# Performance work log

Hardware: AMD Instinct MI355X
Metric: run time of the kernel (lower is better)

Reference implementation:

```python
import jax, jax.numpy as jnp
import numpy as np

N_P, N_A, D, H, E = 200000, 100000, 64, 32, 1000000


def setup_inputs() -> dict:
    key = jax.random.key(0)
    ks = jax.random.split(key, 32)
    inp = {}
    inp["x_paper"] = jax.random.normal(ks[0], (N_P, D), jnp.float32)
    inp["x_author"] = jax.random.normal(ks[1], (N_A, D), jnp.float32)
    inp["cites_src"] = jax.random.randint(ks[2], (E,), 0, N_P, jnp.int32)
    inp["cites_dst"] = jax.random.randint(ks[3], (E,), 0, N_P, jnp.int32)
    inp["writes_src"] = jax.random.randint(ks[4], (E,), 0, N_A, jnp.int32)
    inp["writes_dst"] = jax.random.randint(ks[5], (E,), 0, N_P, jnp.int32)
    inp["rev_src"] = jax.random.randint(ks[6], (E,), 0, N_P, jnp.int32)
    inp["rev_dst"] = jax.random.randint(ks[7], (E,), 0, N_A, jnp.int32)
    # per-relation SAGEConv params; layer 1: D->H, layer 2: H->H
    i = 8
    for layer, din in ((1, D), (2, H)):
        for rel in ("cites", "writes", "rev"):
            inp[f"W{layer}l_{rel}"] = 0.1 * jax.random.normal(ks[i], (din, H), jnp.float32); i += 1
            inp[f"W{layer}r_{rel}"] = 0.1 * jax.random.normal(ks[i], (din, H), jnp.float32); i += 1
            inp[f"b{layer}_{rel}"] = 0.01 * jax.random.normal(ks[i], (H,), jnp.float32); i += 1
    return inp


def _sage(x_src, x_dst, src, dst, Wl, Wr, b, n_dst):
    # PyG SAGEConv (aggr='mean'): lin_l(mean of source msgs) + lin_r(x_dst) + bias
    msg = x_src[src]                                              # [E, d] gather
    s = jax.ops.segment_sum(msg, dst, num_segments=n_dst)         # [n_dst, d]
    cnt = jax.ops.segment_sum(jnp.ones((src.shape[0],), x_src.dtype), dst, num_segments=n_dst)
    mean = s / jnp.maximum(cnt, 1.0)[:, None]
    return mean @ Wl + x_dst @ Wr + b


def reference(x_paper, x_author, cites_src, cites_dst, writes_src, writes_dst,
              rev_src, rev_dst,
              W1l_cites, W1r_cites, b1_cites, W1l_writes, W1r_writes, b1_writes,
              W1l_rev, W1r_rev, b1_rev,
              W2l_cites, W2r_cites, b2_cites, W2l_writes, W2r_writes, b2_writes,
              W2l_rev, W2r_rev, b2_rev):
    n_p, n_a = x_paper.shape[0], x_author.shape[0]
    # layer 1 (to_hetero sums relation outputs per dst node type), then relu
    p1 = jax.nn.relu(
        _sage(x_paper, x_paper, cites_src, cites_dst, W1l_cites, W1r_cites, b1_cites, n_p)
        + _sage(x_author, x_paper, writes_src, writes_dst, W1l_writes, W1r_writes, b1_writes, n_p))
    a1 = jax.nn.relu(
        _sage(x_paper, x_author, rev_src, rev_dst, W1l_rev, W1r_rev, b1_rev, n_a))
    # layer 2, return 'paper' output (no activation)
    p2 = (_sage(p1, p1, cites_src, cites_dst, W2l_cites, W2r_cites, b2_cites, n_p)
          + _sage(a1, p1, writes_src, writes_dst, W2l_writes, W2r_writes, b2_writes, n_p))
    return p2
```

## Files before the change

kernel.cpp:

```cpp
#include <hip/hip_runtime.h>

typedef unsigned short u16;
typedef unsigned int   u32;
typedef __attribute__((ext_vector_type(8))) short bf16x8;
typedef __attribute__((ext_vector_type(4))) float f32x4;

#define N_P 200000
#define N_A 100000
#define DD  64
#define HH  32
#define NE  1000000
#define NBP 782
#define NBA 391
#define NB4K 245
#define NCB 196
#define P4CAP 8192
#define NB_P16 12500
#define NB_A16 6250

__device__ inline float bf2f(u16 u) { return __uint_as_float(((u32)u) << 16); }
__device__ inline u16 f2bf(float f) {
    u32 u = __float_as_uint(f);
    u += 0x7fffu + ((u >> 16) & 1u);
    return (u16)(u >> 16);
}
__device__ inline float lo_f(u32 m) { return __uint_as_float(m << 16); }
__device__ inline float hi_f(u32 m) { return __uint_as_float(m & 0xffff0000u); }

__device__ inline void gseg_dual(
    const u16* __restrict__ yA, const int* __restrict__ bkA, int s0, int e0,
    const u16* __restrict__ yB, const int* __restrict__ bkB, int s1, int e1,
    int lane, float& axo, float& ayo, float& bxo, float& byo) {
    float ax = 0.f, ay = 0.f, bx = 0.f, by = 0.f;
    int lastA = min(max(e0 - 1, s0), NE - 1);
    int lastB = min(max(e1 - 1, s1), NE - 1);
    for (int j0 = s0, j1 = s1; (j0 < e0) || (j1 < e1); j0 += 8, j1 += 8) {
        int ia[8], ib[8];
#pragma unroll
        for (int i = 0; i < 8; ++i) ia[i] = bkA[min(j0 + i, lastA)];
#pragma unroll
        for (int i = 0; i < 8; ++i) ib[i] = bkB[min(j1 + i, lastB)];
        u32 ma[8], mb[8];
#pragma unroll
        for (int i = 0; i < 8; ++i)
            ma[i] = *(const u32*)(yA + (size_t)(u32)ia[i] + lane * 2);
#pragma unroll
        for (int i = 0; i < 8; ++i)
            mb[i] = *(const u32*)(yB + (size_t)(u32)ib[i] + lane * 2);
#pragma unroll
        for (int i = 0; i < 8; ++i) {
            u32 va = (j0 + i < e0) ? ma[i] : 0u;
            ax += lo_f(va); ay += hi_f(va);
        }
#pragma unroll
        for (int i = 0; i < 8; ++i) {
            u32 vb = (j1 + i < e1) ? mb[i] : 0u;
            bx += lo_f(vb); by += hi_f(vb);
        }
    }
    axo = ax; ayo = ay; bxo = bx; byo = by;
}

__global__ __launch_bounds__(256) void p1_hist_k(
    const int* __restrict__ cd, const int* __restrict__ wd, const int* __restrict__ rd,
    int* __restrict__ gsizes) {
    int rel = blockIdx.y;
    const int* dst; int shift;
    if (rel == 0)      { dst = cd; shift = 10; }
    else if (rel == 1) { dst = wd; shift = 10; }
    else               { dst = rd; shift = 9;  }
    __shared__ int cnt[256];
    int t = threadIdx.x;
    cnt[t] = 0;
    __syncthreads();
    int e0 = blockIdx.x * 4096;
    if (e0 + 4096 <= NE) {
        const int4* dv = (const int4*)(dst + e0);
#pragma unroll
        for (int i = 0; i < 4; ++i) {
            int4 v = dv[i * 256 + t];
            atomicAdd(&cnt[v.x >> shift], 1);
            atomicAdd(&cnt[v.y >> shift], 1);
            atomicAdd(&cnt[v.z >> shift], 1);
            atomicAdd(&cnt[v.w >> shift], 1);
        }
    } else {
#pragma unroll
        for (int i = 0; i < 16; ++i) {
            int e = e0 + i * 256 + t;
            if (e < NE) atomicAdd(&cnt[dst[e] >> shift], 1);
        }
    }
    __syncthreads();
    if (t < NCB && cnt[t]) atomicAdd(&gsizes[rel * NCB + t], cnt[t]);
}

__global__ __launch_bounds__(256) void p2_scan_k(
    const int* __restrict__ gsizes, int* __restrict__ bases, int* __restrict__ gcur) {
    __shared__ int lds[256];
    int t = threadIdx.x;
    for (int rel = 0; rel < 3; ++rel) {
        int v = (t < NCB) ? gsizes[rel * NCB + t] : 0;
        lds[t] = v; __syncthreads();
#pragma unroll
        for (int o = 1; o < 256; o <<= 1) {
            int x = (t >= o) ? lds[t - o] : 0;
            __syncthreads();
            lds[t] += x;
            __syncthreads();
        }
        int ex = lds[t] - v;
        if (t < NCB) { bases[rel * NCB + t] = ex; gcur[rel * NCB + t] = ex; }
        __syncthreads();
    }
}

__global__ __launch_bounds__(256) void p3_bin_k(
    const int* __restrict__ cs, const int* __restrict__ cd,
    const int* __restrict__ ws_, const int* __restrict__ wd,
    const int* __restrict__ rs, const int* __restrict__ rd,
    int* __restrict__ gcur,
    u32* __restrict__ pr_c, u32* __restrict__ pr_w, u32* __restrict__ pr_r) {
    int rel = blockIdx.y;
    const int *src, *dst; int shift; u32* out;
    if (rel == 0)      { src = cs;  dst = cd; shift = 10; out = pr_c; }
    else if (rel == 1) { src = ws_; dst = wd; shift = 10; out = pr_w; }
    else               { src = rs;  dst = rd; shift = 9;  out = pr_r; }
    __shared__ u32 sbuf[4096];
    __shared__ int cnt[256], sc[256], lcur[256], gbase[256];
    int t = threadIdx.x;
    cnt[t] = 0;
    __syncthreads();
    int e0 = blockIdx.x * 4096;
    int myd[16], mys[16];
    if (e0 + 4096 <= NE) {
        const int4* dv = (const int4*)(dst + e0);
        const int4* sv = (const int4*)(src + e0);
#pragma unroll
        for (int i = 0; i < 4; ++i) {
            int4 v = dv[i * 256 + t];
            int4 s = sv[i * 256 + t];
            myd[4 * i] = v.x; myd[4 * i + 1] = v.y; myd[4 * i + 2] = v.z; myd[4 * i + 3] = v.w;
            mys[4 * i] = s.x; mys[4 * i + 1] = s.y; mys[4 * i + 2] = s.z; mys[4 * i + 3] = s.w;
            atomicAdd(&cnt[v.x >> shift], 1);
            atomicAdd(&cnt[v.y >> shift], 1);
            atomicAdd(&cnt[v.z >> shift], 1);
            atomicAdd(&cnt[v.w >> shift], 1);
        }
    } else {
#pragma unroll
        for (int i = 0; i < 4; ++i) {
#pragma unroll
            for (int c = 0; c < 4; ++c) {
                int e = e0 + (i * 256 + t) * 4 + c;
                int idx = 4 * i + c;
                if (e < NE) {
                    myd[idx] = dst[e]; mys[idx] = src[e];
                    atomicAdd(&cnt[myd[idx] >> shift], 1);
                } else { myd[idx] = -1; mys[idx] = 0; }
            }
        }
    }
    __syncthreads();
    int v = cnt[t];
    sc[t] = v; __syncthreads();
#pragma unroll
    for (int o = 1; o < 256; o <<= 1) {
        int x = (t >= o) ? sc[t - o] : 0;
        __syncthreads();
        sc[t] += x;
        __syncthreads();
    }
    int ex = sc[t] - v;
    __syncthreads();
    sc[t] = ex;
    lcur[t] = ex;
    if (t < NCB) gbase[t] = atomicAdd(&gcur[rel * NCB + t], cnt[t]);
    __syncthreads();
#pragma unroll
    for (int i = 0; i < 16; ++i) {
        if (myd[i] >= 0) {
            int d = myd[i];
            int cb = d >> shift;
            u32 dloc = (u32)(d - (cb << shift));
            u32 pk = (dloc << 18) | (u32)mys[i];
            int p = atomicAdd(&lcur[cb], 1);
            sbuf[p] = pk;
        }
    }
    __syncthreads();
    int nvalid = min(4096, NE - e0);
    for (int i = t; i < nvalid; i += 256) {
        int lo = 0, hi = NCB - 1;
        while (lo < hi) {
            int mid = (lo + hi + 1) >> 1;
            if (sc[mid] <= i) lo = mid; else hi = mid - 1;
        }
        out[gbase[lo] + (i - sc[lo])] = sbuf[i];
    }
}

__global__ __launch_bounds__(256) void p4_sort_k(
    const int* __restrict__ bases, const int* __restrict__ gsizes,
    const u32* __restrict__ pr_c, const u32* __restrict__ pr_w, const u32* __restrict__ pr_r,
    int* __restrict__ bkt_c, int* __restrict__ bkt_w, int* __restrict__ bkt_r,
    int* __restrict__ st_c, int* __restrict__ st_w, int* __restrict__ st_r) {
    int rel = blockIdx.y;
    const u32* pr; int* bkt; int* st; int width, n;
    if (rel == 0)      { pr = pr_c; bkt = bkt_c; st = st_c; width = 1024; n = N_P; }
    else if (rel == 1) { pr = pr_w; bkt = bkt_w; st = st_w; width = 1024; n = N_P; }
    else               { pr = pr_r; bkt = bkt_r; st = st_r; width = 512;  n = N_A; }
    __shared__ u32 sin[P4CAP];
    __shared__ int cnt[1024], sc2[1024], tmp[256];
    int t = threadIdx.x;
    int b = blockIdx.x;
    int base = bases[rel * NCB + b];
    int size = min(gsizes[rel * NCB + b], P4CAP);
    int d0 = b * width;
    int nd = min(width, n - d0);
    if (nd <= 0) return;
#pragma unroll
    for (int j = t; j < 1024; j += 256) cnt[j] = 0;
    __syncthreads();
    for (int i = t; i < size; i += 256) {
        u32 pk = pr[base + i];
        sin[i] = pk;
        atomicAdd(&cnt[pk >> 18], 1);
    }
    __syncthreads();
    int j0 = 4 * t;
    int c0 = cnt[j0], c1 = cnt[j0 + 1], c2 = cnt[j0 + 2], c3 = cnt[j0 + 3];
    int tot = c0 + c1 + c2 + c3;
    tmp[t] = tot; __syncthreads();
#pragma unroll
    for (int o = 1; o < 256; o <<= 1) {
        int x = (t >= o) ? tmp[t - o] : 0;
        __syncthreads();
        tmp[t] += x;
        __syncthreads();
    }
    int pre = tmp[t] - tot;
    sc2[j0] = pre;
    sc2[j0 + 1] = pre + c0;
    sc2[j0 + 2] = pre + c0 + c1;
    sc2[j0 + 3] = pre + c0 + c1 + c2;
    __syncthreads();
    for (int j = t; j < nd; j += 256) st[d0 + j] = base + sc2[j];
#pragma unroll
    for (int j = t; j < 1024; j += 256) cnt[j] = 0;
    __syncthreads();
    for (int i = t; i < size; i += 256) {
        u32 pk = sin[i];
        int dl = (int)(pk >> 18);
        int pos = sc2[dl] + atomicAdd(&cnt[dl], 1);
        bkt[base + pos] = (int)((pk & 0x3FFFFu) * HH);
    }
}

__global__ __launch_bounds__(256) void prep_w_k(
    const float* __restrict__ W1lc, const float* __restrict__ W1lr,
    const float* __restrict__ W1rc, const float* __restrict__ W1rw,
    const float* __restrict__ W1lw, const float* __restrict__ W1rr,
    const float* __restrict__ W2lc, const float* __restrict__ W2rc,
    const float* __restrict__ W2rw, const float* __restrict__ W2lw,
    const float* __restrict__ b1c, const float* __restrict__ b1w,
    const float* __restrict__ b2c, const float* __restrict__ b2w,
    u16* __restrict__ wt1h, u16* __restrict__ wt1l,
    u16* __restrict__ wt2h, u16* __restrict__ wt2l,
    float* __restrict__ b1s, float* __restrict__ b2s,
    int* __restrict__ gsizes) {
    int m = blockIdx.x, t = threadIdx.x;
    if (m == 0) {
        for (int e = t; e < 3 * NCB; e += 256) gsizes[e] = 0;
    }
    if (m < 5) {
        const float *A = nullptr, *B = nullptr;
        if (m == 0) A = W1lc;
        else if (m == 1) A = W1lr;
        else if (m == 2) { A = W1rc; B = W1rw; }
        else if (m == 3) A = W1lw;
        else A = W1rr;
        for (int e = t; e < 2048; e += 256) {
            int k = e >> 5, n = e & 31;
            float v = A[e] + (B ? B[e] : 0.f);
            u16 h = f2bf(v);
            u16 lw = f2bf(v - bf2f(h));
            wt1h[m * 2048 + n * 64 + k] = h;
            wt1l[m * 2048 + n * 64 + k] = lw;
        }
        if (m == 2 && t < HH) b1s[t] = b1c[t] + b1w[t];
    } else {
        int mm = m - 5;
        const float *A = nullptr, *B = nullptr;
        if (mm == 0) A = W2lc;
        else if (mm == 1) { A = W2rc; B = W2rw; }
        else A = W2lw;
        for (int e = t; e < 1024; e += 256) {
            int k = e >> 5, n = e & 31;
            float v = A[e] + (B ? B[e] : 0.f);
            u16 h = f2bf(v);
            u16 lw = f2bf(v - bf2f(h));
            wt2h[mm * 1024 + n * 32 + k] = h;
            wt2l[mm * 1024 + n * 32 + k] = lw;
        }
        if (mm == 1 && t < HH) b2s[t] = b2c[t] + b2w[t];
    }
}

__global__ __launch_bounds__(256) void t1_k(
    const float* __restrict__ xp, const float* __restrict__ xa,
    const u16* __restrict__ wt1h, const u16* __restrict__ wt1l,
    const float* __restrict__ b1s, const float* __restrict__ b1r,
    u16* __restrict__ y_pc, u16* __restrict__ y_pr, u16* __restrict__ y_aw,
    u16* __restrict__ hb_p, u16* __restrict__ hb_a) {
    __shared__ float Cs[256 * 34];
    int t = threadIdx.x, w = t >> 6, l = t & 63;
    int lm = l & 15, lk = l >> 4;
    bool paper = blockIdx.x < NBP;
    int row0 = (paper ? blockIdx.x : blockIdx.x - NBP) * 256;
    const float* x = paper ? xp : xa;
    int NROW = paper ? N_P : N_A;
    int nv = min(256, NROW - row0);
    bf16x8 xh[4][2], xl[4][2];
#pragma unroll
    for (int i = 0; i < 4; ++i) {
        int rowg = min(row0 + w * 64 + i * 16 + lm, NROW - 1);
        const float* rp = x + (size_t)rowg * DD + lk * 8;
#pragma unroll
        for (int kc = 0; kc < 2; ++kc) {
            float4 a = *(const float4*)(rp + kc * 32);
            float4 b = *(const float4*)(rp + kc * 32 + 4);
            float f[8] = {a.x, a.y, a.z, a.w, b.x, b.y, b.z, b.w};
            union { u32 u[4]; bf16x8 v; } H, L;
#pragma unroll
            for (int j = 0; j < 4; ++j) {
                u16 h0 = f2bf(f[2 * j]), h1 = f2bf(f[2 * j + 1]);
                float l0 = f[2 * j] - bf2f(h0), l1 = f[2 * j + 1] - bf2f(h1);
                H.u[j] = (u32)h0 | ((u32)h1 << 16);
                L.u[j] = (u32)f2bf(l0) | ((u32)f2bf(l1) << 16);
            }
            xh[i][kc] = H.v; xl[i][kc] = L.v;
        }
    }
    int nw = paper ? 3 : 2;
#pragma unroll 1
    for (int iw = 0; iw < nw; ++iw) {
        int mat = paper ? iw : (3 + iw);
        const u16* Wh = wt1h + mat * 2048;
        const u16* Wl = wt1l + mat * 2048;
        bf16x8 Bh[2][2], Bl[2][2];
#pragma unroll
        for (int ct = 0; ct < 2; ++ct)
#pragma unroll
            for (int kc = 0; kc < 2; ++kc) {
                int off = (ct * 16 + lm) * 64 + kc * 32 + lk * 8;
                Bh[ct][kc] = *(const bf16x8*)(Wh + off);
                Bl[ct][kc] = *(const bf16x8*)(Wl + off);
            }
        float bv[2] = {0.f, 0.f};
        if (paper && iw == 2)  { bv[0] = b1s[lm]; bv[1] = b1s[16 + lm]; }
        if (!paper && iw == 1) { bv[0] = b1r[lm]; bv[1] = b1r[16 + lm]; }
#pragma unroll
        for (int i = 0; i < 4; ++i) {
#pragma unroll
            for (int ct = 0; ct < 2; ++ct) {
                f32x4 acc = {bv[ct], bv[ct], bv[ct], bv[ct]};
                acc = __builtin_amdgcn_mfma_f32_16x16x32_bf16(xh[i][0], Bh[ct][0], acc, 0, 0, 0);
                acc = __builtin_amdgcn_mfma_f32_16x16x32_bf16(xh[i][1], Bh[ct][1], acc, 0, 0, 0);
                acc = __builtin_amdgcn_mfma_f32_16x16x32_bf16(xl[i][0], Bh[ct][0], acc, 0, 0, 0);
                acc = __builtin_amdgcn_mfma_f32_16x16x32_bf16(xl[i][1], Bh[ct][1], acc, 0, 0, 0);
                acc = __builtin_amdgcn_mfma_f32_16x16x32_bf16(xh[i][0], Bl[ct][0], acc, 0, 0, 0);
                acc = __builtin_amdgcn_mfma_f32_16x16x32_bf16(xh[i][1], Bl[ct][1], acc, 0, 0, 0);
                int rbase = w * 64 + i * 16 + lk * 4;
#pragma unroll
                for (int r = 0; r < 4; ++r)
                    Cs[(rbase + r) * 34 + ct * 16 + lm] = acc[r];
            }
        }
        asm volatile("s_waitcnt lgkmcnt(0)" ::: "memory");
        u16* outp;
        if (paper) outp = (iw == 0) ? y_pc : (iw == 1) ? y_pr : hb_p;
        else       outp = (iw == 0) ? y_aw : hb_a;
        u32* g = (u32*)(outp + (size_t)row0 * HH);
#pragma unroll
        for (int p = 0; p < 4; ++p) {
            int j = p * 64 + l;
            int rl = w * 64 + (j >> 2);
            if (rl < nv) {
                const float* q = Cs + rl * 34 + (j & 3) * 8;
                u32 o[4];
#pragma unroll
                for (int jj = 0; jj < 4; ++jj)
                    o[jj] = (u32)f2bf(q[2 * jj]) | ((u32)f2bf(q[2 * jj + 1]) << 16);
                *(uint4*)(g + ((size_t)w * 256 + j) * 4) = make_uint4(o[0], o[1], o[2], o[3]);
            }
        }
        asm volatile("" ::: "memory");
    }
}

__global__ __launch_bounds__(256) void agg1_k(
    const u16* __restrict__ y_pc, const u16* __restrict__ y_aw,
    const u16* __restrict__ y_pr,
    const int* __restrict__ st_c, const int* __restrict__ bkt_c,
    const int* __restrict__ st_w, const int* __restrict__ bkt_w,
    const int* __restrict__ st_r, const int* __restrict__ bkt_r,
    u32* __restrict__ hb_p, u32* __restrict__ hb_a) {
    int t = threadIdx.x, g = t >> 4, lane = t & 15;
    if (blockIdx.x < NB_P16) {
        int row = blockIdx.x * 16 + g;
        int s0 = st_c[row];
        int e0 = (row == N_P - 1) ? NE : st_c[row + 1];
        int s1 = st_w[row];
        int e1 = (row == N_P - 1) ? NE : st_w[row + 1];
        float cx, cy, wx, wy;
        gseg_dual(y_pc, bkt_c, s0, e0, y_aw, bkt_w, s1, e1, lane, cx, cy, wx, wy);
        int d0 = e0 - s0, d1 = e1 - s1;
        float iv0 = 1.0f / (float)(d0 < 1 ? 1 : d0);
        float iv1 = 1.0f / (float)(d1 < 1 ? 1 : d1);
        u32 self = hb_p[(size_t)row * (HH / 2) + lane];
        float ax = cx * iv0 + wx * iv1 + lo_f(self);
        float ay = cy * iv0 + wy * iv1 + hi_f(self);
        hb_p[(size_t)row * (HH / 2) + lane] = (u32)f2bf(ax) | ((u32)f2bf(ay) << 16);
    } else {
        int row = (blockIdx.x - NB_P16) * 16 + g;
        int s = st_r[row];
        int e = (row == N_A - 1) ? NE : st_r[row + 1];
        int mid = (s + e) >> 1;
        float ax0, ay0, ax1, ay1;
        gseg_dual(y_pr, bkt_r, s, mid, y_pr, bkt_r, mid, e, lane, ax0, ay0, ax1, ay1);
        int dg = e - s;
        float iv = 1.0f / (float)(dg < 1 ? 1 : dg);
        u32 self = hb_a[(size_t)row * (HH / 2) + lane];
        float ax = (ax0 + ax1) * iv + lo_f(self);
        float ay = (ay0 + ay1) * iv + hi_f(self);
        hb_a[(size_t)row * (HH / 2) + lane] = (u32)f2bf(ax) | ((u32)f2bf(ay) << 16);
    }
}

__global__ __launch_bounds__(256) void t2_k(
    const u32* __restrict__ hb_p, const u32* __restrict__ hb_a,
    const u16* __restrict__ wt2h, const u16* __restrict__ wt2l,
    const float* __restrict__ b2s,
    u16* __restrict__ z_p, u16* __restrict__ z_a, float* __restrict__ hp2) {
    __shared__ float Cs[256 * 34];
    int t = threadIdx.x, w = t >> 6, l = t & 63;
    int lm = l & 15, lk = l >> 4;
    bool paper = blockIdx.x < NBP;
    int row0 = (paper ? blockIdx.x : blockIdx.x - NBP) * 256;
    const u32* hb = paper ? hb_p : hb_a;
    int NROW = paper ? N_P : N_A;
    int nv = min(256, NROW - row0);
    bf16x8 af[4];
#pragma unroll
    for (int i = 0; i < 4; ++i) {
        int rowg = min(row0 + w * 64 + i * 16 + lm, NROW - 1);
        uint4 q = *(const uint4*)(hb + (size_t)rowg * (HH / 2) + lk * 4);
        u32 qq[4] = {q.x, q.y, q.z, q.w};
        union { u32 u[4]; bf16x8 v; } A;
#pragma unroll
        for (int j = 0; j < 4; ++j) {
            u32 m = ((qq[j] & 0x80008000u) >> 15) * 0xFFFFu;
            A.u[j] = qq[j] & ~m;
        }
        af[i] = A.v;
    }
    int nw = paper ? 2 : 1;
#pragma unroll 1
    for (int iw = 0; iw < nw; ++iw) {
        int mat = paper ? iw : 2;
        const u16* Wh = wt2h + mat * 1024;
        const u16* Wl = wt2l + mat * 1024;
        bf16x8 Bh[2], Bl[2];
#pragma unroll
        for (int ct = 0; ct < 2; ++ct) {
            int off = (ct * 16 + lm) * 32 + lk * 8;
            Bh[ct] = *(const bf16x8*)(Wh + off);
            Bl[ct] = *(const bf16x8*)(Wl + off);
        }
        float bv[2] = {0.f, 0.f};
        if (paper && iw == 1) { bv[0] = b2s[lm]; bv[1] = b2s[16 + lm]; }
#pragma unroll
        for (int i = 0; i < 4; ++i) {
#pragma unroll
            for (int ct = 0; ct < 2; ++ct) {
                f32x4 acc = {bv[ct], bv[ct], bv[ct], bv[ct]};
                acc = __builtin_amdgcn_mfma_f32_16x16x32_bf16(af[i], Bh[ct], acc, 0, 0, 0);
                acc = __builtin_amdgcn_mfma_f32_16x16x32_bf16(af[i], Bl[ct], acc, 0, 0, 0);
                int rbase = w * 64 + i * 16 + lk * 4;
#pragma unroll
                for (int r = 0; r < 4; ++r)
                    Cs[(rbase + r) * 34 + ct * 16 + lm] = acc[r];
            }
        }
        asm volatile("s_waitcnt lgkmcnt(0)" ::: "memory");
        if (paper && iw == 1) {
            float* gf = hp2 + (size_t)row0 * HH;
#pragma unroll
            for (int p = 0; p < 8; ++p) {
                int j = p * 64 + l;
                int rl = w * 64 + (j >> 3);
                if (rl < nv) {
                    const float* q = Cs + rl * 34 + (j & 7) * 4;
                    *(float4*)(gf + ((size_t)w * 512 + j) * 4) =
                        make_float4(q[0], q[1], q[2], q[3]);
                }
            }
        } else {
            u16* outp = paper ? z_p : z_a;
            u32* g = (u32*)(outp + (size_t)row0 * HH);
#pragma unroll
            for (int p = 0; p < 4; ++p) {
                int j = p * 64 + l;
                int rl = w * 64 + (j >> 2);
                if (rl < nv) {
                    const float* q = Cs + rl * 34 + (j & 3) * 8;
                    u32 o[4];
#pragma unroll
                    for (int jj = 0; jj < 4; ++jj)
                        o[jj] = (u32)f2bf(q[2 * jj]) | ((u32)f2bf(q[2 * jj + 1]) << 16);
                    *(uint4*)(g + ((size_t)w * 256 + j) * 4) = make_uint4(o[0], o[1], o[2], o[3]);
                }
            }
        }
        asm volatile("" ::: "memory");
    }
}

__global__ __launch_bounds__(256) void agg2_k(
    const u16* __restrict__ z_p, const u16* __restrict__ z_a,
    const int* __restrict__ st_c, const int* __restrict__ bkt_c,
    const int* __restrict__ st_w, const int* __restrict__ bkt_w,
    const float* __restrict__ hp2, float* __restrict__ out) {
    int t = threadIdx.x, g = t >> 4, lane = t & 15;
    int row = blockIdx.x * 16 + g;
    int s0 = st_c[row];
    int e0 = (row == N_P - 1) ? NE : st_c[row + 1];
    int s1 = st_w[row];
    int e1 = (row == N_P - 1) ? NE : st_w[row + 1];
    float cx, cy, wx, wy;
    gseg_dual(z_p, bkt_c, s0, e0, z_a, bkt_w, s1, e1, lane, cx, cy, wx, wy);
    int d0 = e0 - s0, d1 = e1 - s1;
    float iv0 = 1.0f / (float)(d0 < 1 ? 1 : d0);
    float iv1 = 1.0f / (float)(d1 < 1 ? 1 : d1);
    float2 h = *(const float2*)(hp2 + (size_t)row * HH + lane * 2);
    float2 o = make_float2(h.x + cx * iv0 + wx * iv1,
                           h.y + cy * iv0 + wy * iv1);
    *(float2*)(out + (size_t)row * HH + lane * 2) = o;
}

extern "C" void kernel_launch(void* const* d_in, const int* in_sizes, int n_in,
                              void* d_out, int out_size, void* d_ws, size_t ws_size,
                              hipStream_t stream) {
    const float* x_p  = (const float*)d_in[0];
    const float* x_a  = (const float*)d_in[1];
    const int* c_src  = (const int*)d_in[2];
    const int* c_dst  = (const int*)d_in[3];
    const int* w_src  = (const int*)d_in[4];
    const int* w_dst  = (const int*)d_in[5];
    const int* r_src  = (const int*)d_in[6];
    const int* r_dst  = (const int*)d_in[7];
    const float* W1l_c = (const float*)d_in[8];
    const float* W1r_c = (const float*)d_in[9];
    const float* b1_c  = (const float*)d_in[10];
    const float* W1l_w = (const float*)d_in[11];
    const float* W1r_w = (const float*)d_in[12];
    const float* b1_w  = (const float*)d_in[13];
    const float* W1l_r = (const float*)d_in[14];
    const float* W1r_r = (const float*)d_in[15];
    const float* b1_r  = (const float*)d_in[16];
    const float* W2l_c = (const float*)d_in[17];
    const float* W2r_c = (const float*)d_in[18];
    const float* b2_c  = (const float*)d_in[19];
    const float* W2l_w = (const float*)d_in[20];
    const float* W2r_w = (const float*)d_in[21];
    const float* b2_w  = (const float*)d_in[22];

    int* gsizes = (int*)d_ws;
    int* bases  = gsizes + 3 * NCB;
    int* gcur   = bases + 3 * NCB;
    int* st_c   = gcur + 3 * NCB;
    int* st_w   = st_c + N_P;
    int* st_r   = st_w + N_P;
    int* bkt_c  = st_r + N_A;
    int* bkt_w  = bkt_c + NE;
    int* bkt_r  = bkt_w + NE;
    u16* wt1h  = (u16*)(bkt_r + NE);
    u16* wt1l  = wt1h + 5 * 2048;
    u16* wt2h  = wt1l + 5 * 2048;
    u16* wt2l  = wt2h + 3 * 1024;
    float* b1s = (float*)(wt2l + 3 * 1024);
    float* b2s = b1s + HH;
    u16* hb_p  = (u16*)(b2s + HH);
    u16* hb_a  = hb_p + (size_t)N_P * HH;
    u16* y_pc  = hb_a + (size_t)N_A * HH;
    u16* y_pr  = y_pc + (size_t)N_P * HH;
    u16* y_aw  = y_pr + (size_t)N_P * HH;
    float* hp2 = (float*)(y_aw + (size_t)N_A * HH);
    u32* pr_c  = (u32*)hp2;
    u32* pr_w  = pr_c + NE;
    u32* pr_r  = pr_w + NE;
    u16* z_p   = y_pc;
    u16* z_a   = y_aw;
    float* outp = (float*)d_out;

    const size_t need = ((uintptr_t)(hp2 + (size_t)N_P * HH)) - (uintptr_t)d_ws;
    if (ws_size < need) return;

    prep_w_k<<<8, 256, 0, stream>>>(W1l_c, W1l_r, W1r_c, W1r_w, W1l_w, W1r_r,
                                    W2l_c, W2r_c, W2r_w, W2l_w,
                                    b1_c, b1_w, b2_c, b2_w,
                                    wt1h, wt1l, wt2h, wt2l, b1s, b2s, gsizes);
    p1_hist_k<<<dim3(NB4K, 3), 256, 0, stream>>>(c_dst, w_dst, r_dst, gsizes);
    p2_scan_k<<<1, 256, 0, stream>>>(gsizes, bases, gcur);
    p3_bin_k<<<dim3(NB4K, 3), 256, 0, stream>>>(c_src, c_dst, w_src, w_dst, r_src, r_dst,
                                                gcur, pr_c, pr_w, pr_r);
    p4_sort_k<<<dim3(NCB, 3), 256, 0, stream>>>(bases, gsizes, pr_c, pr_w, pr_r,
                                                bkt_c, bkt_w, bkt_r, st_c, st_w, st_r);
    t1_k<<<NBP + NBA, 256, 0, stream>>>(x_p, x_a, wt1h, wt1l, b1s, b1_r,
                                        y_pc, y_pr, y_aw, hb_p, hb_a);
    agg1_k<<<NB_P16 + NB_A16, 256, 0, stream>>>(y_pc, y_aw, y_pr,
                                                st_c, bkt_c, st_w, bkt_w, st_r, bkt_r,
                                                (u32*)hb_p, (u32*)hb_a);
    t2_k<<<NBP + NBA, 256, 0, stream>>>((const u32*)hb_p, (const u32*)hb_a,
                                        wt2h, wt2l, b2s, z_p, z_a, hp2);
    agg2_k<<<NB_P16, 256, 0, stream>>>(z_p, z_a, st_c, bkt_c, st_w, bkt_w, hp2, outp);
}
```

Before: 395.3 us.

## Fuse edge binning with layer-1 transform kernel and use hardware bf16 pack

Merges the edge-binning scatter kernel and the layer-1 dense transform into one launch, with blocks split by index, so the independent work runs concurrently and one launch is dropped. The binning scatter now records each entry's bucket id in a byte array instead of binary-searching the prefix array. Software bf16 rounding is replaced by the v_cvt_pk_bf16_f32 instruction in several kernels, and the x high part is formed by truncation. Self-row loads in the aggregation kernels are hoisted earlier to overlap with the gathers. Risks include slightly different bf16 hi/lo split numerics and a larger shared-memory footprint for the binning blocks.

Measured after the change: 373.7 us. -5.4%, faster.

```diff
diff --git a/kernel.cpp b/kernel.cpp
--- a/kernel.cpp
+++ b/kernel.cpp
@@ -2,6 +2,7 @@
 
 typedef unsigned short u16;
 typedef unsigned int   u32;
+typedef unsigned char  u8;
 typedef __attribute__((ext_vector_type(8))) short bf16x8;
 typedef __attribute__((ext_vector_type(4))) float f32x4;
 
@@ -17,6 +18,7 @@
 #define P4CAP 8192
 #define NB_P16 12500
 #define NB_A16 6250
+#define NB4K3 735
 
 __device__ inline float bf2f(u16 u) { return __uint_as_float(((u32)u) << 16); }
 __device__ inline u16 f2bf(float f) {
@@ -26,6 +28,11 @@
 }
 __device__ inline float lo_f(u32 m) { return __uint_as_float(m << 16); }
 __device__ inline float hi_f(u32 m) { return __uint_as_float(m & 0xffff0000u); }
+__device__ inline u32 cvtpk(float a, float b) {
+    u32 r;
+    asm("v_cvt_pk_bf16_f32 %0, %1, %2" : "=v"(r) : "v"(a), "v"(b));
+    return r;
+}
 
 __device__ inline void gseg_dual(
     const u16* __restrict__ yA, const int* __restrict__ bkA, int s0, int e0,
@@ -115,88 +122,188 @@
     }
 }
 
-__global__ __launch_bounds__(256) void p3_bin_k(
+__global__ __launch_bounds__(256) void p3t1_k(
     const int* __restrict__ cs, const int* __restrict__ cd,
     const int* __restrict__ ws_, const int* __restrict__ wd,
     const int* __restrict__ rs, const int* __restrict__ rd,
     int* __restrict__ gcur,
-    u32* __restrict__ pr_c, u32* __restrict__ pr_w, u32* __restrict__ pr_r) {
-    int rel = blockIdx.y;
-    const int *src, *dst; int shift; u32* out;
-    if (rel == 0)      { src = cs;  dst = cd; shift = 10; out = pr_c; }
-    else if (rel == 1) { src = ws_; dst = wd; shift = 10; out = pr_w; }
-    else               { src = rs;  dst = rd; shift = 9;  out = pr_r; }
-    __shared__ u32 sbuf[4096];
-    __shared__ int cnt[256], sc[256], lcur[256], gbase[256];
+    u32* __restrict__ pr_c, u32* __restrict__ pr_w, u32* __restrict__ pr_r,
+    const float* __restrict__ xp, const float* __restrict__ xa,
+    const u16* __restrict__ wt1h, const u16* __restrict__ wt1l,
+    const float* __restrict__ b1s, const float* __restrict__ b1r,
+    u16* __restrict__ y_pc, u16* __restrict__ y_pr, u16* __restrict__ y_aw,
+    u16* __restrict__ hb_p, u16* __restrict__ hb_a) {
+    __shared__ float smem[256 * 34];
     int t = threadIdx.x;
-    cnt[t] = 0;
-    __syncthreads();
-    int e0 = blockIdx.x * 4096;
-    int myd[16], mys[16];
-    if (e0 + 4096 <= NE) {
-        const int4* dv = (const int4*)(dst + e0);
-        const int4* sv = (const int4*)(src + e0);
+    if (blockIdx.x < NB4K3) {
+        u32* sbuf  = (u32*)smem;
+        int* cnt   = (int*)(smem + 4096);
+        int* sc    = (int*)(smem + 4352);
+        int* lcur  = (int*)(smem + 4608);
+        int* gbase = (int*)(smem + 4864);
+        u8*  bb    = (u8*)(smem + 5120);
+        int rel = blockIdx.x / NB4K;
+        int blk = blockIdx.x - rel * NB4K;
+        const int *src, *dst; int shift; u32* out;
+        if (rel == 0)      { src = cs;  dst = cd; shift = 10; out = pr_c; }
+        else if (rel == 1) { src = ws_; dst = wd; shift = 10; out = pr_w; }
+        else               { src = rs;  dst = rd; shift = 9;  out = pr_r; }
+        cnt[t] = 0;
+        __syncthreads();
+        int e0 = blk * 4096;
+        int myd[16], mys[16];
+        if (e0 + 4096 <= NE) {
+            const int4* dv = (const int4*)(dst + e0);
+            const int4* sv = (const int4*)(src + e0);
+#pragma unroll
+            for (int i = 0; i < 4; ++i) {
+                int4 v = dv[i * 256 + t];
+                int4 s = sv[i * 256 + t];
+                myd[4 * i] = v.x; myd[4 * i + 1] = v.y; myd[4 * i + 2] = v.z; myd[4 * i + 3] = v.w;
+                mys[4 * i] = s.x; mys[4 * i + 1] = s.y; mys[4 * i + 2] = s.z; mys[4 * i + 3] = s.w;
+                atomicAdd(&cnt[v.x >> shift], 1);
+                atomicAdd(&cnt[v.y >> shift], 1);
+                atomicAdd(&cnt[v.z >> shift], 1);
+                atomicAdd(&cnt[v.w >> shift], 1);
+            }
+        } else {
+#pragma unroll
+            for (int i = 0; i < 4; ++i) {
+#pragma unroll
+                for (int c = 0; c < 4; ++c) {
+                    int e = e0 + (i * 256 + t) * 4 + c;
+                    int idx = 4 * i + c;
+                    if (e < NE) {
+                        myd[idx] = dst[e]; mys[idx] = src[e];
+                        atomicAdd(&cnt[myd[idx] >> shift], 1);
+                    } else { myd[idx] = -1; mys[idx] = 0; }
+                }
+            }
+        }
+        __syncthreads();
+        int v = cnt[t];
+        sc[t] = v; __syncthreads();
+#pragma unroll
+        for (int o = 1; o < 256; o <<= 1) {
+            int x = (t >= o) ? sc[t - o] : 0;
+            __syncthreads();
+            sc[t] += x;
+            __syncthreads();
+        }
+        int ex = sc[t] - v;
+        __syncthreads();
+        sc[t] = ex;
+        lcur[t] = ex;
+        if (t < NCB) gbase[t] = atomicAdd(&gcur[rel * NCB + t], cnt[t]);
+        __syncthreads();
+#pragma unroll
+        for (int i = 0; i < 16; ++i) {
+            if (myd[i] >= 0) {
+                int d = myd[i];
+                int cb = d >> shift;
+                u32 dloc = (u32)(d - (cb << shift));
+                u32 pk = (dloc << 18) | (u32)mys[i];
+                int p = atomicAdd(&lcur[cb], 1);
+                sbuf[p] = pk;
+                bb[p] = (u8)cb;
+            }
+        }
+        __syncthreads();
+        int nvalid = min(4096, NE - e0);
+        for (int i = t; i < nvalid; i += 256) {
+            int cb = bb[i];
+            out[gbase[cb] + (i - sc[cb])] = sbuf[i];
+        }
+    } else {
+        float* Cs = smem;
+        int w = t >> 6, l = t & 63;
+        int lm = l & 15, lk = l >> 4;
+        int bx = blockIdx.x - NB4K3;
+        bool paper = bx < NBP;
+        int row0 = (paper ? bx : bx - NBP) * 256;
+        const float* x = paper ? xp : xa;
+        int NROW = paper ? N_P : N_A;
+        int nv = min(256, NROW - row0);
+        bf16x8 xh[4][2], xl[4][2];
 #pragma unroll
         for (int i = 0; i < 4; ++i) {
-            int4 v = dv[i * 256 + t];
-            int4 s = sv[i * 256 + t];
-            myd[4 * i] = v.x; myd[4 * i + 1] = v.y; myd[4 * i + 2] = v.z; myd[4 * i + 3] = v.w;
-            mys[4 * i] = s.x; mys[4 * i + 1] = s.y; mys[4 * i + 2] = s.z; mys[4 * i + 3] = s.w;
-            atomicAdd(&cnt[v.x >> shift], 1);
-            atomicAdd(&cnt[v.y >> shift], 1);
-            atomicAdd(&cnt[v.z >> shift], 1);
-            atomicAdd(&cnt[v.w >> shift], 1);
-        }
-    } else {
-#pragma unroll
-        for (int i = 0; i < 4; ++i) {
-#pragma unroll
-            for (int c = 0; c < 4; ++c) {
-                int e = e0 + (i * 256 + t) * 4 + c;
-                int idx = 4 * i + c;
-                if (e < NE) {
-                    myd[idx] = dst[e]; mys[idx] = src[e];
-                    atomicAdd(&cnt[myd[idx] >> shift], 1);
-                } else { myd[idx] = -1; mys[idx] = 0; }
-            }
-        }
-    }
-    __syncthreads();
-    int v = cnt[t];
-    sc[t] = v; __syncthreads();
-#pragma unroll
-    for (int o = 1; o < 256; o <<= 1) {
-        int x = (t >= o) ? sc[t - o] : 0;
-        __syncthreads();
-        sc[t] += x;
-        __syncthreads();
-    }
-    int ex = sc[t] - v;
-    __syncthreads();
-    sc[t] = ex;
-    lcur[t] = ex;
-    if (t < NCB) gbase[t] = atomicAdd(&gcur[rel * NCB + t], cnt[t]);
-    __syncthreads();
-#pragma unroll
-    for (int i = 0; i < 16; ++i) {
-        if (myd[i] >= 0) {
-            int d = myd[i];
-            int cb = d >> shift;
-            u32 dloc = (u32)(d - (cb << shift));
-            u32 pk = (dloc << 18) | (u32)mys[i];
-            int p = atomicAdd(&lcur[cb], 1);
-            sbuf[p] = pk;
-        }
-    }
-    __syncthreads();
-    int nvalid = min(4096, NE - e0);
-    for (int i = t; i < nvalid; i += 256) {
-        int lo = 0, hi = NCB - 1;
-        while (lo < hi) {
-            int mid = (lo + hi + 1) >> 1;
-            if (sc[mid] <= i) lo = mid; else hi = mid - 1;
-        }
-        out[gbase[lo] + (i - sc[lo])] = sbuf[i];
+            int rowg = min(row0 + w * 64 + i * 16 + lm, NROW - 1);
+            const float* rp = x + (size_t)rowg * DD + lk * 8;
+#pragma unroll
+            for (int kc = 0; kc < 2; ++kc) {
+                float4 a = *(const float4*)(rp + kc * 32);
+                float4 b = *(const float4*)(rp + kc * 32 + 4);
+                float f[8] = {a.x, a.y, a.z, a.w, b.x, b.y, b.z, b.w};
+                union { u32 u[4]; bf16x8 v; } H, L;
+#pragma unroll
+                for (int j = 0; j < 4; ++j) {
+                    u32 u0 = __float_as_uint(f[2 * j]);
+                    u32 u1 = __float_as_uint(f[2 * j + 1]);
+                    u32 m0 = u0 & 0xffff0000u;
+                    u32 m1 = u1 & 0xffff0000u;
+                    H.u[j] = (u0 >> 16) | m1;
+                    float l0 = f[2 * j]     - __uint_as_float(m0);
+                    float l1 = f[2 * j + 1] - __uint_as_float(m1);
+                    L.u[j] = cvtpk(l0, l1);
+                }
+                xh[i][kc] = H.v; xl[i][kc] = L.v;
+            }
+        }
+        int nw = paper ? 3 : 2;
+#pragma unroll 1
+        for (int iw = 0; iw < nw; ++iw) {
+            int mat = paper ? iw : (3 + iw);
+            const u16* Wh = wt1h + mat * 2048;
+            const u16* Wl = wt1l + mat * 2048;
+            bf16x8 Bh[2][2], Bl[2][2];
+#pragma unroll
+            for (int ct = 0; ct < 2; ++ct)
+#pragma unroll
+                for (int kc = 0; kc < 2; ++kc) {
+                    int off = (ct * 16 + lm) * 64 + kc * 32 + lk * 8;
+                    Bh[ct][kc] = *(const bf16x8*)(Wh + off);
+                    Bl[ct][kc] = *(const bf16x8*)(Wl + off);
+                }
+            float bv[2] = {0.f, 0.f};
+            if (paper && iw == 2)  { bv[0] = b1s[lm]; bv[1] = b1s[16 + lm]; }
+            if (!paper && iw == 1) { bv[0] = b1r[lm]; bv[1] = b1r[16 + lm]; }
+#pragma unroll
+            for (int i = 0; i < 4; ++i) {
+#pragma unroll
+                for (int ct = 0; ct < 2; ++ct) {
+                    f32x4 acc = {bv[ct], bv[ct], bv[ct], bv[ct]};
+                    acc = __builtin_amdgcn_mfma_f32_16x16x32_bf16(xh[i][0], Bh[ct][0], acc, 0, 0, 0);
+                    acc = __builtin_amdgcn_mfma_f32_16x16x32_bf16(xh[i][1], Bh[ct][1], acc, 0, 0, 0);
+                    acc = __builtin_amdgcn_mfma_f32_16x16x32_bf16(xl[i][0], Bh[ct][0], acc, 0, 0, 0);
+                    acc = __builtin_amdgcn_mfma_f32_16x16x32_bf16(xl[i][1], Bh[ct][1], acc, 0, 0, 0);
+                    acc = __builtin_amdgcn_mfma_f32_16x16x32_bf16(xh[i][0], Bl[ct][0], acc, 0, 0, 0);
+                    acc = __builtin_amdgcn_mfma_f32_16x16x32_bf16(xh[i][1], Bl[ct][1], acc, 0, 0, 0);
+                    int rbase = w * 64 + i * 16 + lk * 4;
+#pragma unroll
+                    for (int r = 0; r < 4; ++r)
+                        Cs[(rbase + r) * 34 + ct * 16 + lm] = acc[r];
+                }
+            }
+            asm volatile("s_waitcnt lgkmcnt(0)" ::: "memory");
+            u16* outp;
+            if (paper) outp = (iw == 0) ? y_pc : (iw == 1) ? y_pr : hb_p;
+            else       outp = (iw == 0) ? y_aw : hb_a;
+            u32* g = (u32*)(outp + (size_t)row0 * HH);
+#pragma unroll
+            for (int p = 0; p < 4; ++p) {
+                int j = p * 64 + l;
+                int rl = w * 64 + (j >> 2);
+                if (rl < nv) {
+                    const float* q = Cs + rl * 34 + (j & 3) * 8;
+                    u32 o[4];
+#pragma unroll
+                    for (int jj = 0; jj < 4; ++jj)
+                        o[jj] = cvtpk(q[2 * jj], q[2 * jj + 1]);
+                    *(uint4*)(g + ((size_t)w * 256 + j) * 4) = make_uint4(o[0], o[1], o[2], o[3]);
+                }
+            }
+            asm volatile("" ::: "memory");
+        }
     }
 }
 
@@ -307,98 +414,6 @@
     }
 }
 
-__global__ __launch_bounds__(256) void t1_k(
-    const float* __restrict__ xp, const float* __restrict__ xa,
-    const u16* __restrict__ wt1h, const u16* __restrict__ wt1l,
-    const float* __restrict__ b1s, const float* __restrict__ b1r,
-    u16* __restrict__ y_pc, u16* __restrict__ y_pr, u16* __restrict__ y_aw,
-    u16* __restrict__ hb_p, u16* __restrict__ hb_a) {
-    __shared__ float Cs[256 * 34];
-    int t = threadIdx.x, w = t >> 6, l = t & 63;
-    int lm = l & 15, lk = l >> 4;
-    bool paper = blockIdx.x < NBP;
-    int row0 = (paper ? blockIdx.x : blockIdx.x - NBP) * 256;
-    const float* x = paper ? xp : xa;
-    int NROW = paper ? N_P : N_A;
-    int nv = min(256, NROW - row0);
-    bf16x8 xh[4][2], xl[4][2];
-#pragma unroll
-    for (int i = 0; i < 4; ++i) {
-        int rowg = min(row0 + w * 64 + i * 16 + lm, NROW - 1);
-        const float* rp = x + (size_t)rowg * DD + lk * 8;
-#pragma unroll
-        for (int kc = 0; kc < 2; ++kc) {
-            float4 a = *(const float4*)(rp + kc * 32);
-            float4 b = *(const float4*)(rp + kc * 32 + 4);
-            float f[8] = {a.x, a.y, a.z, a.w, b.x, b.y, b.z, b.w};
-            union { u32 u[4]; bf16x8 v; } H, L;
-#pragma unroll
-            for (int j = 0; j < 4; ++j) {
-                u16 h0 = f2bf(f[2 * j]), h1 = f2bf(f[2 * j + 1]);
-                float l0 = f[2 * j] - bf2f(h0), l1 = f[2 * j + 1] - bf2f(h1);
-                H.u[j] = (u32)h0 | ((u32)h1 << 16);
-                L.u[j] = (u32)f2bf(l0) | ((u32)f2bf(l1) << 16);
-            }
-            xh[i][kc] = H.v; xl[i][kc] = L.v;
-        }
-    }
-    int nw = paper ? 3 : 2;
-#pragma unroll 1
-    for (int iw = 0; iw < nw; ++iw) {
-        int mat = paper ? iw : (3 + iw);
-        const u16* Wh = wt1h + mat * 2048;
-        const u16* Wl = wt1l + mat * 2048;
-        bf16x8 Bh[2][2], Bl[2][2];
-#pragma unroll
-        for (int ct = 0; ct < 2; ++ct)
-#pragma unroll
-            for (int kc = 0; kc < 2; ++kc) {
-                int off = (ct * 16 + lm) * 64 + kc * 32 + lk * 8;
-                Bh[ct][kc] = *(const bf16x8*)(Wh + off);
-                Bl[ct][kc] = *(const bf16x8*)(Wl + off);
-            }
-        float bv[2] = {0.f, 0.f};
-        if (paper && iw == 2)  { bv[0] = b1s[lm]; bv[1] = b1s[16 + lm]; }
-        if (!paper && iw == 1) { bv[0] = b1r[lm]; bv[1] = b1r[16 + lm]; }
-#pragma unroll
-        for (int i = 0; i < 4; ++i) {
-#pragma unroll
-            for (int ct = 0; ct < 2; ++ct) {
-                f32x4 acc = {bv[ct], bv[ct], bv[ct], bv[ct]};
-                acc = __builtin_amdgcn_mfma_f32_16x16x32_bf16(xh[i][0], Bh[ct][0], acc, 0, 0, 0);
-                acc = __builtin_amdgcn_mfma_f32_16x16x32_bf16(xh[i][1], Bh[ct][1], acc, 0, 0, 0);
-                acc = __builtin_amdgcn_mfma_f32_16x16x32_bf16(xl[i][0], Bh[ct][0], acc, 0, 0, 0);
-                acc = __builtin_amdgcn_mfma_f32_16x16x32_bf16(xl[i][1], Bh[ct][1], acc, 0, 0, 0);
-                acc = __builtin_amdgcn_mfma_f32_16x16x32_bf16(xh[i][0], Bl[ct][0], acc, 0, 0, 0);
-                acc = __builtin_amdgcn_mfma_f32_16x16x32_bf16(xh[i][1], Bl[ct][1], acc, 0, 0, 0);
-                int rbase = w * 64 + i * 16 + lk * 4;
-#pragma unroll
-                for (int r = 0; r < 4; ++r)
-                    Cs[(rbase + r) * 34 + ct * 16 + lm] = acc[r];
-            }
-        }
-        asm volatile("s_waitcnt lgkmcnt(0)" ::: "memory");
-        u16* outp;
-        if (paper) outp = (iw == 0) ? y_pc : (iw == 1) ? y_pr : hb_p;
-        else       outp = (iw == 0) ? y_aw : hb_a;
-        u32* g = (u32*)(outp + (size_t)row0 * HH);
-#pragma unroll
-        for (int p = 0; p < 4; ++p) {
-            int j = p * 64 + l;
-            int rl = w * 64 + (j >> 2);
-            if (rl < nv) {
-                const float* q = Cs + rl * 34 + (j & 3) * 8;
-                u32 o[4];
-#pragma unroll
-                for (int jj = 0; jj < 4; ++jj)
-                    o[jj] = (u32)f2bf(q[2 * jj]) | ((u32)f2bf(q[2 * jj + 1]) << 16);
-                *(uint4*)(g + ((size_t)w * 256 + j) * 4) = make_uint4(o[0], o[1], o[2], o[3]);
-            }
-        }
-        asm volatile("" ::: "memory");
-    }
-}
-
 __global__ __launch_bounds__(256) void agg1_k(
     const u16* __restrict__ y_pc, const u16* __restrict__ y_aw,
     const u16* __restrict__ y_pr,
@@ -409,6 +424,7 @@
     int t = threadIdx.x, g = t >> 4, lane = t & 15;
     if (blockIdx.x < NB_P16) {
         int row = blockIdx.x * 16 + g;
+        u32 self = hb_p[(size_t)row * (HH / 2) + lane];
         int s0 = st_c[row];
         int e0 = (row == N_P - 1) ? NE : st_c[row + 1];
         int s1 = st_w[row];
@@ -418,12 +434,12 @@
         int d0 = e0 - s0, d1 = e1 - s1;
         float iv0 = 1.0f / (float)(d0 < 1 ? 1 : d0);
         float iv1 = 1.0f / (float)(d1 < 1 ? 1 : d1);
-        u32 self = hb_p[(size_t)row * (HH / 2) + lane];
         float ax = cx * iv0 + wx * iv1 + lo_f(self);
         float ay = cy * iv0 + wy * iv1 + hi_f(self);
-        hb_p[(size_t)row * (HH / 2) + lane] = (u32)f2bf(ax) | ((u32)f2bf(ay) << 16);
+        hb_p[(size_t)row * (HH / 2) + lane] = cvtpk(ax, ay);
     } else {
         int row = (blockIdx.x - NB_P16) * 16 + g;
+        u32 self = hb_a[(size_t)row * (HH / 2) + lane];
         int s = st_r[row];
         int e = (row == N_A - 1) ? NE : st_r[row + 1];
         int mid = (s + e) >> 1;
@@ -431,10 +447,9 @@
         gseg_dual(y_pr, bkt_r, s, mid, y_pr, bkt_r, mid, e, lane, ax0, ay0, ax1, ay1);
         int dg = e - s;
         float iv = 1.0f / (float)(dg < 1 ? 1 : dg);
-        u32 self = hb_a[(size_t)row * (HH / 2) + lane];
         float ax = (ax0 + ax1) * iv + lo_f(self);
         float ay = (ay0 + ay1) * iv + hi_f(self);
-        hb_a[(size_t)row * (HH / 2) + lane] = (u32)f2bf(ax) | ((u32)f2bf(ay) << 16);
+        hb_a[(size_t)row * (HH / 2) + lane] = cvtpk(ax, ay);
     }
 }
 
@@ -518,7 +533,7 @@
                     u32 o[4];
 #pragma unroll
                     for (int jj = 0; jj < 4; ++jj)
-                        o[jj] = (u32)f2bf(q[2 * jj]) | ((u32)f2bf(q[2 * jj + 1]) << 16);
+                        o[jj] = cvtpk(q[2 * jj], q[2 * jj + 1]);
                     *(uint4*)(g + ((size_t)w * 256 + j) * 4) = make_uint4(o[0], o[1], o[2], o[3]);
                 }
             }
@@ -534,6 +549,7 @@
     const float* __restrict__ hp2, float* __restrict__ out) {
     int t = threadIdx.x, g = t >> 4, lane = t & 15;
     int row = blockIdx.x * 16 + g;
+    float2 h = *(const float2*)(hp2 + (size_t)row * HH + lane * 2);
     int s0 = st_c[row];
     int e0 = (row == N_P - 1) ? NE : st_c[row + 1];
     int s1 = st_w[row];
@@ -543,7 +559,6 @@
     int d0 = e0 - s0, d1 = e1 - s1;
     float iv0 = 1.0f / (float)(d0 < 1 ? 1 : d0);
     float iv1 = 1.0f / (float)(d1 < 1 ? 1 : d1);
-    float2 h = *(const float2*)(hp2 + (size_t)row * HH + lane * 2);
     float2 o = make_float2(h.x + cx * iv0 + wx * iv1,
                            h.y + cy * iv0 + wy * iv1);
     *(float2*)(out + (size_t)row * HH + lane * 2) = o;
@@ -613,12 +628,11 @@
                                     wt1h, wt1l, wt2h, wt2l, b1s, b2s, gsizes);
     p1_hist_k<<<dim3(NB4K, 3), 256, 0, stream>>>(c_dst, w_dst, r_dst, gsizes);
     p2_scan_k<<<1, 256, 0, stream>>>(gsizes, bases, gcur);
-    p3_bin_k<<<dim3(NB4K, 3), 256, 0, stream>>>(c_src, c_dst, w_src, w_dst, r_src, r_dst,
-                                                gcur, pr_c, pr_w, pr_r);
+    p3t1_k<<<NB4K3 + NBP + NBA, 256, 0, stream>>>(
+        c_src, c_dst, w_src, w_dst, r_src, r_dst, gcur, pr_c, pr_w, pr_r,
+        x_p, x_a, wt1h, wt1l, b1s, b1_r, y_pc, y_pr, y_aw, hb_p, hb_a);
     p4_sort_k<<<dim3(NCB, 3), 256, 0, stream>>>(bases, gsizes, pr_c, pr_w, pr_r,
                                                 bkt_c, bkt_w, bkt_r, st_c, st_w, st_r);
-    t1_k<<<NBP + NBA, 256, 0, stream>>>(x_p, x_a, wt1h, wt1l, b1s, b1_r,
-                                        y_pc, y_pr, y_aw, hb_p, hb_a);
     agg1_k<<<NB_P16 + NB_A16, 256, 0, stream>>>(y_pc, y_aw, y_pr,
                                                 st_c, bkt_c, st_w, bkt_w, st_r, bkt_r,
                                                 (u32*)hb_p, (u32*)hb_a);
```
